# Optimization experiments

Measured on AMD Instinct MI355X. Metric: run time of the kernel, lower is better.

The kernel has to match this reference:

```python
import jax, jax.numpy as jnp
import numpy as np

EPS = 1.1920929e-07  # torch F.rms_norm default eps for fp32
HEADS = 16
KV_HEADS = 4
HEAD_DIM = 64
WINDOW = 1024
NEG = -1e30

def rms_norm(x):
    return x * jax.lax.rsqrt(jnp.mean(x * x, axis=-1, keepdims=True) + EPS)

def rope_freqs(L, head_dim):
    half = head_dim // 2
    inv_freq = 1.0 / (10000.0 ** (jnp.arange(half, dtype=jnp.float32) / half))
    f = jnp.outer(jnp.arange(L, dtype=jnp.float32), inv_freq)  # (L, half)
    return jnp.concatenate([f, f], axis=-1)  # (L, head_dim)

def apply_rope(x, freqs):
    # x: (B, L, H, D), freqs: (L, D)
    cos = jnp.cos(freqs)[None, :, None, :]
    sin = jnp.sin(freqs)[None, :, None, :]
    half = x.shape[-1] // 2
    x1, x2 = x[..., :half], x[..., half:]
    return jnp.concatenate([
        x1 * cos[..., :half] - x2 * sin[..., half:],
        x1 * sin[..., :half] + x2 * cos[..., half:],
    ], axis=-1)

def setup_inputs() -> dict:
    key = jax.random.key(0)
    k1, k2, k3, k4 = jax.random.split(key, 4)
    B, L, D = 2, 2048, 1024
    x = jax.random.normal(k1, (B, L, D), dtype=jnp.float32)
    w_qkv = jax.random.normal(k2, (1536, D), dtype=jnp.float32) * 0.02
    w_out = jax.random.normal(k3, (D, D), dtype=jnp.float32) * 0.02
    reset_mask = jax.random.randint(k4, (B, L), 0, 2) == 1
    return {"x": x, "w_qkv": w_qkv, "w_out": w_out, "reset_mask": reset_mask}

def reference(x, w_qkv, w_out, reset_mask):
    B, L, D = x.shape
    residual = x
    h = rms_norm(x)
    qkv = h @ w_qkv.T  # (B, L, 1536)
    q_dim = HEADS * HEAD_DIM
    kv_dim = KV_HEADS * HEAD_DIM
    q = qkv[..., :q_dim].reshape(B, L, HEADS, HEAD_DIM)
    k = qkv[..., q_dim:q_dim + kv_dim].reshape(B, L, KV_HEADS, HEAD_DIM)
    v = qkv[..., q_dim + kv_dim:].reshape(B, L, KV_HEADS, HEAD_DIM)
    q = rms_norm(q)
    k = rms_norm(k)
    freqs = rope_freqs(L, HEAD_DIM)
    q = apply_rope(q, freqs)
    k = apply_rope(k, freqs)
    groups = HEADS // KV_HEADS
    k = jnp.repeat(k, groups, axis=2)  # (B, L, H, D)
    v = jnp.repeat(v, groups, axis=2)
    q = q.transpose(0, 2, 1, 3)  # (B, H, L, D)
    k = k.transpose(0, 2, 1, 3)
    v = v.transpose(0, 2, 1, 3)
    # mask: same document & causal & sliding window
    seg = jnp.cumsum(reset_mask.astype(jnp.int32), axis=1)  # (B, L)
    same_doc = seg[:, :, None] == seg[:, None, :]  # (B, L, L)
    idx = jnp.arange(L)
    dist = idx[:, None] - idx[None, :]
    cw = (dist >= 0) & (dist < WINDOW)  # (L, L)
    mask = same_doc & cw[None]  # (B, L, L)
    scale = 1.0 / np.sqrt(HEAD_DIM)
    scores = jnp.einsum('bhqd,bhkd->bhqk', q, k) * scale
    scores = jnp.where(mask[:, None, :, :], scores, NEG)
    probs = jax.nn.softmax(scores, axis=-1)
    y = jnp.einsum('bhqk,bhkd->bhqd', probs, v)
    y = y.transpose(0, 2, 1, 3).reshape(B, L, D)
    return residual + y @ w_out.T
```

## Files before the change

### kernel.cpp

```cpp
#include <hip/hip_runtime.h>

typedef __attribute__((ext_vector_type(8))) short short8;
typedef __attribute__((ext_vector_type(4))) float f32x4;
typedef __attribute__((ext_vector_type(4))) unsigned short us4;

typedef unsigned int __attribute__((address_space(3))) lds_u32;
typedef const unsigned int __attribute__((address_space(1))) glb_u32;

__device__ __forceinline__ unsigned short f2bf(float f){
  unsigned int u = __float_as_uint(f);
  u = (u + 0x7FFFu + ((u >> 16) & 1u)) >> 16;
  return (unsigned short)u;
}
__device__ __forceinline__ float bf2f(unsigned short h){
  return __uint_as_float(((unsigned int)h) << 16);
}

__global__ __launch_bounds__(256)
void prep(const float* __restrict__ wq, const float* __restrict__ wo,
          unsigned short* __restrict__ wqb, unsigned short* __restrict__ wob,
          const float* __restrict__ x, unsigned short* __restrict__ h,
          const unsigned char* __restrict__ mb, int* __restrict__ lo){
  int blk = blockIdx.x;
  int t = threadIdx.x;
  if (blk < 2560) {
    int i = blk * 256 + t;
    const int n1 = 1536 * 1024 / 4;
    float4 v = (i < n1) ? ((const float4*)wq)[i] : ((const float4*)wo)[i - n1];
    us4 o = { f2bf(v.x), f2bf(v.y), f2bf(v.z), f2bf(v.w) };
    if (i < n1) ((us4*)wqb)[i] = o;
    else        ((us4*)wob)[i - n1] = o;
    return;
  }
  if (blk < 2560 + 4096) {
    int row = blk - 2560;
    float4 v = ((const float4*)(x + (size_t)row * 1024))[t];
    float ss = v.x*v.x + v.y*v.y + v.z*v.z + v.w*v.w;
    #pragma unroll
    for (int m = 1; m < 64; m <<= 1) ss += __shfl_xor(ss, m);
    __shared__ float wsum[4];
    if ((t & 63) == 0) wsum[t >> 6] = ss;
    __syncthreads();
    float tot = wsum[0] + wsum[1] + wsum[2] + wsum[3];
    float sc = rsqrtf(tot * (1.f/1024.f) + 1.1920929e-07f);
    us4 o = { f2bf(v.x*sc), f2bf(v.y*sc), f2bf(v.z*sc), f2bf(v.w*sc) };
    *(us4*)(h + (size_t)row * 1024 + t * 4) = o;
    return;
  }
  int b = blk - 2560 - 4096;
  __shared__ int flag_s;
  if (t == 0) flag_s = 0;
  __syncthreads();
  if (t < 64 && (t & 3) != 0 && mb[t] != 0) atomicOr(&flag_s, 1);
  __syncthreads();
  const bool isb = (flag_s != 0);
  const int* mi = (const int*)mb;
  int tmax = 0;
  int mvals[8];
  #pragma unroll
  for (int j = 0; j < 8; j++) {
    int p = t * 8 + j;
    int mv = isb ? (int)mb[b*2048 + p] : mi[b*2048 + p];
    mvals[j] = mv;
    if (mv) tmax = p;
  }
  __shared__ int sm[256];
  sm[t] = tmax;
  __syncthreads();
  for (int offd = 1; offd < 256; offd <<= 1) {
    int v = (t >= offd) ? sm[t - offd] : 0;
    __syncthreads();
    if (t >= offd) sm[t] = max(sm[t], v);
    __syncthreads();
  }
  int run = (t > 0) ? sm[t - 1] : 0;
  #pragma unroll
  for (int j = 0; j < 8; j++) {
    int p = t * 8 + j;
    if (mvals[j]) run = p;
    int l = run, wlo = p - 1023;
    if (wlo > l) l = wlo;
    if (l < 0) l = 0;
    lo[b*2048 + p] = l;
  }
}

template<bool BF_OUT, bool RES>
__global__ __launch_bounds__(256)
void gemm_nt(const unsigned short* __restrict__ A, const unsigned short* __restrict__ B,
             int M, int N, int K, float* __restrict__ Cf, unsigned short* __restrict__ Cb,
             const float* __restrict__ resid){
  __shared__ __align__(16) short As[128 * 64];
  __shared__ __align__(16) short Bs[128 * 64];
  const int nbn = N >> 7;
  const int bm = blockIdx.x / nbn;
  const int bn = blockIdx.x % nbn;
  const int t = threadIdx.x;
  const int lane = t & 63;
  const int wv = t >> 6;
  const int wm = (wv >> 1) * 64, wn = (wv & 1) * 64;
  const int lr = lane & 15, lg = lane >> 4;
  const int l8 = lane >> 3;
  const int c8 = (lane & 7) * 8;

  f32x4 acc[4][4];
  #pragma unroll
  for (int m = 0; m < 4; m++)
    #pragma unroll
    for (int n = 0; n < 4; n++) acc[m][n] = (f32x4){0.f,0.f,0.f,0.f};

  const unsigned short* Ab = A + (size_t)(bm * 128) * K;
  const unsigned short* Bb = B + (size_t)(bn * 128) * K;

  for (int kt = 0; kt < K; kt += 64) {
    #pragma unroll
    for (int i = 0; i < 4; i++) {
      int chunk = wv * 4 + i;
      int row = chunk * 8 + l8;
      __builtin_amdgcn_global_load_lds((glb_u32*)(Ab + (size_t)row * K + kt + c8),
                                       (lds_u32*)&As[chunk * 512], 16, 0, 0);
      __builtin_amdgcn_global_load_lds((glb_u32*)(Bb + (size_t)row * K + kt + c8),
                                       (lds_u32*)&Bs[chunk * 512], 16, 0, 0);
    }
    __syncthreads();
    #pragma unroll
    for (int kk = 0; kk < 2; kk++) {
      short8 af[4], bfr[4];
      #pragma unroll
      for (int m = 0; m < 4; m++) af[m] = *(const short8*)&As[(wm + m*16 + lr)*64 + kk*32 + lg*8];
      #pragma unroll
      for (int n = 0; n < 4; n++) bfr[n] = *(const short8*)&Bs[(wn + n*16 + lr)*64 + kk*32 + lg*8];
      #pragma unroll
      for (int m = 0; m < 4; m++)
        #pragma unroll
        for (int n = 0; n < 4; n++)
          acc[m][n] = __builtin_amdgcn_mfma_f32_16x16x32_bf16(af[m], bfr[n], acc[m][n], 0, 0, 0);
    }
    __syncthreads();
  }
  #pragma unroll
  for (int m = 0; m < 4; m++)
    #pragma unroll
    for (int n = 0; n < 4; n++)
      #pragma unroll
      for (int r = 0; r < 4; r++) {
        int grow = bm*128 + wm + m*16 + lg*4 + r;
        int gcol = bn*128 + wn + n*16 + lr;
        size_t idx = (size_t)grow * N + gcol;
        if (BF_OUT) { Cb[idx] = f2bf(acc[m][n][r]); }
        else {
          float v = acc[m][n][r];
          if (RES) v += resid[idx];
          Cf[idx] = v;
        }
      }
}

__global__ __launch_bounds__(256)
void post_qkv(const unsigned short* __restrict__ qkv,
              unsigned short* __restrict__ Qb, unsigned short* __restrict__ Kb,
              unsigned short* __restrict__ Vt){
  int w = blockIdx.x * 4 + (threadIdx.x >> 6);
  int lane = threadIdx.x & 63;
  int head = w % 24;
  int row  = w / 24;
  int b = row >> 11, pos = row & 2047;
  int off = head < 16 ? head * 64 : (head < 20 ? 1024 + (head-16)*64 : 1280 + (head-20)*64);
  float val = bf2f(qkv[(size_t)row * 1536 + off + lane]);
  if (head < 20) {
    float ss = val * val;
    #pragma unroll
    for (int m = 1; m < 64; m <<= 1) ss += __shfl_xor(ss, m);
    val *= rsqrtf(ss * (1.f/64.f) + 1.1920929e-07f);
    float part = __shfl_xor(val, 32);
    int i = lane & 31;
    float f = (float)pos * exp2f((float)i * (-13.287712379549449f / 32.f));
    float s, c; sincosf(f, &s, &c);
    val = (lane < 32) ? (val * c - part * s) : (part * s + val * c);
  }
  unsigned short o = f2bf(val);
  if (head < 16)      Qb[((size_t)((b*16 + head     )*2048 + pos))*64 + lane] = o;
  else if (head < 20) Kb[((size_t)((b*4  + head - 16)*2048 + pos))*64 + lane] = o;
  else                Vt[((size_t)((b*4  + head - 20)*64 + lane))*2048 + pos] = o;
}

__global__ __launch_bounds__(256)
void attn(const unsigned short* __restrict__ Qb, const unsigned short* __restrict__ Kb,
          const unsigned short* __restrict__ Vt, const int* __restrict__ lo,
          unsigned short* __restrict__ Y){
  int blk = blockIdx.x;
  int qt = blk & 31, h = (blk >> 5) & 15, b = blk >> 9;
  int wv = threadIdx.x >> 6, lane = threadIdx.x & 63;
  int lr = lane & 15, lg = lane >> 4;
  int q0 = qt * 64 + wv * 16;
  const unsigned short* Qh = Qb + ((size_t)(b*16 + h)) * 2048 * 64;
  int kvh = h >> 2;
  const unsigned short* Kh = Kb + ((size_t)(b*4 + kvh)) * 2048 * 64;
  const unsigned short* Vh = Vt + ((size_t)(b*4 + kvh)) * 64 * 2048;
  short8 qa0 = *(const short8*)(Qh + (size_t)(q0 + lr) * 64 + lg * 8);
  short8 qa1 = *(const short8*)(Qh + (size_t)(q0 + lr) * 64 + 32 + lg * 8);
  const int* lop = lo + b * 2048 + q0;
  int4 mlv = *(const int4*)(lop + lg * 4);
  int mylo[4] = {mlv.x, mlv.y, mlv.z, mlv.w};
  int kc0 = lop[0] & ~31;
  int kend = q0 + 15;
  f32x4 oacc[4];
  #pragma unroll
  for (int n = 0; n < 4; n++) oacc[n] = (f32x4){0.f,0.f,0.f,0.f};
  float den[4] = {0.f,0.f,0.f,0.f};
  __shared__ __align__(16) short Pl[4][16 * 40];
  short* Pw = Pl[wv];
  for (int kc = kc0; kc <= kend; kc += 32) {
    f32x4 s[2];
    #pragma unroll
    for (int n = 0; n < 2; n++) {
      int kr = kc + n*16 + lr;
      int krl = min(kr, 2047);
      short8 k0 = *(const short8*)(Kh + (size_t)krl * 64 + lg * 8);
      short8 k1 = *(const short8*)(Kh + (size_t)krl * 64 + 32 + lg * 8);
      f32x4 z = (f32x4){0.f,0.f,0.f,0.f};
      z = __builtin_amdgcn_mfma_f32_16x16x32_bf16(qa0, k0, z, 0, 0, 0);
      z = __builtin_amdgcn_mfma_f32_16x16x32_bf16(qa1, k1, z, 0, 0, 0);
      s[n] = z;
    }
    #pragma unroll
    for (int n = 0; n < 2; n++)
      #pragma unroll
      for (int r = 0; r < 4; r++) {
        int krow = kc + n*16 + lr;
        int qrow = q0 + lg*4 + r;
        bool valid = (krow >= mylo[r]) && (krow <= qrow);
        float p = valid ? __expf(s[n][r] * 0.125f) : 0.f;
        den[r] += p;
        Pw[(lg*4 + r) * 40 + n*16 + lr] = (short)f2bf(p);
      }
    short8 pa = *(const short8*)&Pw[lr * 40 + lg * 8];
    int vc = min(kc + lg * 8, 2040);
    #pragma unroll
    for (int n = 0; n < 4; n++) {
      short8 vb = *(const short8*)(Vh + (size_t)(n*16 + lr) * 2048 + vc);
      oacc[n] = __builtin_amdgcn_mfma_f32_16x16x32_bf16(pa, vb, oacc[n], 0, 0, 0);
    }
  }
  #pragma unroll
  for (int r = 0; r < 4; r++)
    #pragma unroll
    for (int m = 1; m < 16; m <<= 1) den[r] += __shfl_xor(den[r], m);
  #pragma unroll
  for (int n = 0; n < 4; n++)
    #pragma unroll
    for (int r = 0; r < 4; r++) {
      int qrow = q0 + lg*4 + r;
      Y[((size_t)(b*2048 + qrow)) * 1024 + h*64 + n*16 + lr] = f2bf(oacc[n][r] / den[r]);
    }
}

extern "C" void kernel_launch(void* const* d_in, const int* in_sizes, int n_in,
                              void* d_out, int out_size, void* d_ws, size_t ws_size,
                              hipStream_t stream){
  const float* x    = (const float*)d_in[0];
  const float* wqkv = (const float*)d_in[1];
  const float* wout = (const float*)d_in[2];
  const unsigned char* mask = (const unsigned char*)d_in[3];
  float* out = (float*)d_out;
  char* ws = (char*)d_ws;
  size_t off = 0;
  auto alloc = [&](size_t bytes) -> void* {
    void* p = ws + off;
    off += (bytes + 255) & ~(size_t)255;
    return p;
  };
  unsigned short* wq_b  = (unsigned short*)alloc((size_t)1536*1024*2);
  unsigned short* wo_b  = (unsigned short*)alloc((size_t)1024*1024*2);
  unsigned short* h_b   = (unsigned short*)alloc((size_t)4096*1024*2);
  unsigned short* qkv_b = (unsigned short*)alloc((size_t)4096*1536*2);
  unsigned short* q_b   = (unsigned short*)alloc((size_t)4096*1024*2);
  unsigned short* k_b   = (unsigned short*)alloc((size_t)4096*256*2);
  unsigned short* vt_b  = (unsigned short*)alloc((size_t)4096*256*2);
  unsigned short* y_b   = (unsigned short*)alloc((size_t)4096*1024*2);
  int* lo               = (int*)alloc((size_t)4096*4);

  prep<<<2560 + 4096 + 2, 256, 0, stream>>>(wqkv, wout, wq_b, wo_b, x, h_b, mask, lo);
  gemm_nt<true,  false><<<32*12, 256, 0, stream>>>(h_b, wq_b, 4096, 1536, 1024, nullptr, qkv_b, nullptr);
  post_qkv<<<24576, 256, 0, stream>>>(qkv_b, q_b, k_b, vt_b);
  attn<<<1024, 256, 0, stream>>>(q_b, k_b, vt_b, lo, y_b);
  gemm_nt<false, true><<<32*8, 256, 0, stream>>>(y_b, wo_b, 4096, 1024, 1024, out, nullptr, x);
}
```

Before: 164.8 us.

## Fuse QK norm, RoPE and V transpose into pipelined 128x64 QKV GEMM epilogue

Replaces the 128x128 GEMM with a 128x64-tile GEMM that double-buffers LDS loads with explicit waitcnt/barrier scheduling, adds an occupancy hint and swizzles block order. The QKV GEMM epilogue now applies per-head RMS norm and RoPE directly and writes Q/K in head-major layout and V transposed through a swizzled LDS buffer. This removes the separate post_qkv kernel and the intermediate qkv buffer round trip. The smaller tiles raise block count, but each block reuses less data and the epilogue does more work, including a per-row sincos.

```diff
diff --git a/kernel.cpp b/kernel.cpp
--- a/kernel.cpp
+++ b/kernel.cpp
@@ -85,103 +85,154 @@
   }
 }
 
-template<bool BF_OUT, bool RES>
-__global__ __launch_bounds__(256)
-void gemm_nt(const unsigned short* __restrict__ A, const unsigned short* __restrict__ B,
-             int M, int N, int K, float* __restrict__ Cf, unsigned short* __restrict__ Cb,
-             const float* __restrict__ resid){
-  __shared__ __align__(16) short As[128 * 64];
-  __shared__ __align__(16) short Bs[128 * 64];
-  const int nbn = N >> 7;
-  const int bm = blockIdx.x / nbn;
-  const int bn = blockIdx.x % nbn;
-  const int t = threadIdx.x;
-  const int lane = t & 63;
-  const int wv = t >> 6;
-  const int wm = (wv >> 1) * 64, wn = (wv & 1) * 64;
+template<int MODE>
+__global__ __launch_bounds__(256, 3)
+void gemm64(const unsigned short* __restrict__ A, const unsigned short* __restrict__ Bw,
+            unsigned short* __restrict__ Qb, unsigned short* __restrict__ Kb,
+            unsigned short* __restrict__ Vt, float* __restrict__ Cf,
+            const float* __restrict__ resid){
+  constexpr int K = 1024;
+  constexpr int NBN = (MODE == 0) ? 24 : 16;
+  __shared__ __align__(16) short As[2][128 * 64];
+  __shared__ __align__(16) short Bs[2][64 * 64];
+  const int cpx = (NBN * 32) >> 3;
+  const int swz = (blockIdx.x & 7) * cpx + (blockIdx.x >> 3);
+  const int bm = swz / NBN, bn = swz % NBN;
+  const int t = threadIdx.x, lane = t & 63, wv = t >> 6;
   const int lr = lane & 15, lg = lane >> 4;
-  const int l8 = lane >> 3;
-  const int c8 = (lane & 7) * 8;
-
-  f32x4 acc[4][4];
-  #pragma unroll
-  for (int m = 0; m < 4; m++)
+  const int l8 = lane >> 3, c8 = (lane & 7) * 8;
+  const int wr0 = wv * 32;
+
+  f32x4 acc[2][4];
+  #pragma unroll
+  for (int m = 0; m < 2; m++)
     #pragma unroll
     for (int n = 0; n < 4; n++) acc[m][n] = (f32x4){0.f,0.f,0.f,0.f};
 
   const unsigned short* Ab = A + (size_t)(bm * 128) * K;
-  const unsigned short* Bb = B + (size_t)(bn * 128) * K;
-
-  for (int kt = 0; kt < K; kt += 64) {
-    #pragma unroll
-    for (int i = 0; i < 4; i++) {
-      int chunk = wv * 4 + i;
-      int row = chunk * 8 + l8;
-      __builtin_amdgcn_global_load_lds((glb_u32*)(Ab + (size_t)row * K + kt + c8),
-                                       (lds_u32*)&As[chunk * 512], 16, 0, 0);
-      __builtin_amdgcn_global_load_lds((glb_u32*)(Bb + (size_t)row * K + kt + c8),
-                                       (lds_u32*)&Bs[chunk * 512], 16, 0, 0);
-    }
-    __syncthreads();
+  const unsigned short* Bb = Bw + (size_t)(bn * 64) * K;
+
+  #define STAGE(buf, kt) do { \
+    _Pragma("unroll") \
+    for (int i = 0; i < 6; i++) { \
+      int c = wv * 6 + i; \
+      if (c < 16) { \
+        __builtin_amdgcn_global_load_lds((glb_u32*)(Ab + (size_t)(c*8 + l8) * K + (kt) + c8), \
+                                         (lds_u32*)&As[buf][c * 512], 16, 0, 0); \
+      } else { \
+        __builtin_amdgcn_global_load_lds((glb_u32*)(Bb + (size_t)((c-16)*8 + l8) * K + (kt) + c8), \
+                                         (lds_u32*)&Bs[buf][(c-16) * 512], 16, 0, 0); \
+      } \
+    } \
+  } while (0)
+
+  auto COMPUTE = [&](int buf) {
     #pragma unroll
     for (int kk = 0; kk < 2; kk++) {
-      short8 af[4], bfr[4];
-      #pragma unroll
-      for (int m = 0; m < 4; m++) af[m] = *(const short8*)&As[(wm + m*16 + lr)*64 + kk*32 + lg*8];
-      #pragma unroll
-      for (int n = 0; n < 4; n++) bfr[n] = *(const short8*)&Bs[(wn + n*16 + lr)*64 + kk*32 + lg*8];
-      #pragma unroll
-      for (int m = 0; m < 4; m++)
+      short8 af[2], bfr[4];
+      #pragma unroll
+      for (int m = 0; m < 2; m++) af[m] = *(const short8*)&As[buf][(wr0 + m*16 + lr)*64 + kk*32 + lg*8];
+      #pragma unroll
+      for (int n = 0; n < 4; n++) bfr[n] = *(const short8*)&Bs[buf][(n*16 + lr)*64 + kk*32 + lg*8];
+      #pragma unroll
+      for (int m = 0; m < 2; m++)
         #pragma unroll
         for (int n = 0; n < 4; n++)
           acc[m][n] = __builtin_amdgcn_mfma_f32_16x16x32_bf16(af[m], bfr[n], acc[m][n], 0, 0, 0);
     }
+  };
+
+  const int nt = K >> 6;
+  STAGE(0, 0);
+  #pragma unroll 1
+  for (int tt = 0; tt < nt - 1; ++tt) {
+    int cur = tt & 1;
+    STAGE(cur ^ 1, (tt + 1) * 64);
+    __builtin_amdgcn_sched_barrier(0);
+    asm volatile("s_waitcnt vmcnt(6)" ::: "memory");
+    __builtin_amdgcn_s_barrier();
+    __builtin_amdgcn_sched_barrier(0);
+    COMPUTE(cur);
+    __builtin_amdgcn_sched_barrier(0);
+    __builtin_amdgcn_s_barrier();
+  }
+  asm volatile("s_waitcnt vmcnt(0)" ::: "memory");
+  __builtin_amdgcn_s_barrier();
+  __builtin_amdgcn_sched_barrier(0);
+  COMPUTE((nt - 1) & 1);
+  #undef STAGE
+
+  if constexpr (MODE == 1) {
+    #pragma unroll
+    for (int m = 0; m < 2; m++)
+      #pragma unroll
+      for (int n = 0; n < 4; n++)
+        #pragma unroll
+        for (int r = 0; r < 4; r++) {
+          int grow = bm*128 + wr0 + m*16 + lg*4 + r;
+          int gcol = bn*64 + n*16 + lr;
+          size_t idx = (size_t)grow * 1024 + gcol;
+          Cf[idx] = acc[m][n][r] + resid[idx];
+        }
+  } else if (bn < 20) {
+    const float cexp = -13.287712379549449f / 32.f;
+    const float if0 = exp2f((float)lr * cexp);
+    const float if1 = exp2f((float)(lr + 16) * cexp);
+    #pragma unroll
+    for (int m = 0; m < 2; m++)
+      #pragma unroll
+      for (int r = 0; r < 4; r++) {
+        float rs = acc[m][0][r]*acc[m][0][r] + acc[m][1][r]*acc[m][1][r]
+                 + acc[m][2][r]*acc[m][2][r] + acc[m][3][r]*acc[m][3][r];
+        #pragma unroll
+        for (int msk = 1; msk < 16; msk <<= 1) rs += __shfl_xor(rs, msk);
+        float sc = rsqrtf(rs * (1.f/64.f) + 1.1920929e-07f);
+        int grow = bm*128 + wr0 + m*16 + lg*4 + r;
+        int b = grow >> 11, pos = grow & 2047;
+        float th0 = (float)pos * if0, th1 = (float)pos * if1;
+        float s0, c0, s1, c1;
+        sincosf(th0, &s0, &c0);
+        sincosf(th1, &s1, &c1);
+        float v0 = acc[m][0][r]*sc, v1 = acc[m][1][r]*sc;
+        float v2 = acc[m][2][r]*sc, v3 = acc[m][3][r]*sc;
+        float o0 = v0*c0 - v2*s0;
+        float o1 = v1*c1 - v3*s1;
+        float o2 = v2*c0 + v0*s0;
+        float o3 = v3*c1 + v1*s1;
+        unsigned short* dst = (bn < 16)
+          ? Qb + ((size_t)((b*16 + bn)      * 2048 + pos)) * 64
+          : Kb + ((size_t)((b*4  + bn - 16) * 2048 + pos)) * 64;
+        dst[lr]      = f2bf(o0);
+        dst[16 + lr] = f2bf(o1);
+        dst[32 + lr] = f2bf(o2);
+        dst[48 + lr] = f2bf(o3);
+      }
+  } else {
+    short* Vl = &As[0][0];
+    #pragma unroll
+    for (int m = 0; m < 2; m++)
+      #pragma unroll
+      for (int n = 0; n < 4; n++)
+        #pragma unroll
+        for (int r = 0; r < 4; r++) {
+          int pl = wr0 + m*16 + lg*4 + r;
+          int d = n*16 + lr;
+          Vl[pl * 64 + (d ^ ((pl & 7) << 3))] = (short)f2bf(acc[m][n][r]);
+        }
     __syncthreads();
-  }
-  #pragma unroll
-  for (int m = 0; m < 4; m++)
-    #pragma unroll
-    for (int n = 0; n < 4; n++)
-      #pragma unroll
-      for (int r = 0; r < 4; r++) {
-        int grow = bm*128 + wm + m*16 + lg*4 + r;
-        int gcol = bn*128 + wn + n*16 + lr;
-        size_t idx = (size_t)grow * N + gcol;
-        if (BF_OUT) { Cb[idx] = f2bf(acc[m][n][r]); }
-        else {
-          float v = acc[m][n][r];
-          if (RES) v += resid[idx];
-          Cf[idx] = v;
-        }
-      }
-}
-
-__global__ __launch_bounds__(256)
-void post_qkv(const unsigned short* __restrict__ qkv,
-              unsigned short* __restrict__ Qb, unsigned short* __restrict__ Kb,
-              unsigned short* __restrict__ Vt){
-  int w = blockIdx.x * 4 + (threadIdx.x >> 6);
-  int lane = threadIdx.x & 63;
-  int head = w % 24;
-  int row  = w / 24;
-  int b = row >> 11, pos = row & 2047;
-  int off = head < 16 ? head * 64 : (head < 20 ? 1024 + (head-16)*64 : 1280 + (head-20)*64);
-  float val = bf2f(qkv[(size_t)row * 1536 + off + lane]);
-  if (head < 20) {
-    float ss = val * val;
-    #pragma unroll
-    for (int m = 1; m < 64; m <<= 1) ss += __shfl_xor(ss, m);
-    val *= rsqrtf(ss * (1.f/64.f) + 1.1920929e-07f);
-    float part = __shfl_xor(val, 32);
-    int i = lane & 31;
-    float f = (float)pos * exp2f((float)i * (-13.287712379549449f / 32.f));
-    float s, c; sincosf(f, &s, &c);
-    val = (lane < 32) ? (val * c - part * s) : (part * s + val * c);
-  }
-  unsigned short o = f2bf(val);
-  if (head < 16)      Qb[((size_t)((b*16 + head     )*2048 + pos))*64 + lane] = o;
-  else if (head < 20) Kb[((size_t)((b*4  + head - 16)*2048 + pos))*64 + lane] = o;
-  else                Vt[((size_t)((b*4  + head - 20)*64 + lane))*2048 + pos] = o;
+    int vh = bn - 20;
+    int b = bm >> 4;
+    int posg = (bm & 15) * 128;
+    int pl = (t & 63) * 2, dbase = (t >> 6) * 16;
+    #pragma unroll
+    for (int dd = 0; dd < 16; dd++) {
+      int d = dbase + dd;
+      unsigned short w0 = (unsigned short)Vl[pl * 64 + (d ^ ((pl & 7) << 3))];
+      unsigned short w1 = (unsigned short)Vl[(pl+1) * 64 + (d ^ (((pl+1) & 7) << 3))];
+      unsigned int pk = (unsigned int)w0 | ((unsigned int)w1 << 16);
+      *(unsigned int*)(Vt + ((size_t)((b*4 + vh)*64 + d)) * 2048 + posg + pl) = pk;
+    }
+  }
 }
 
 __global__ __launch_bounds__(256)
@@ -273,7 +324,6 @@
   unsigned short* wq_b  = (unsigned short*)alloc((size_t)1536*1024*2);
   unsigned short* wo_b  = (unsigned short*)alloc((size_t)1024*1024*2);
   unsigned short* h_b   = (unsigned short*)alloc((size_t)4096*1024*2);
-  unsigned short* qkv_b = (unsigned short*)alloc((size_t)4096*1536*2);
   unsigned short* q_b   = (unsigned short*)alloc((size_t)4096*1024*2);
   unsigned short* k_b   = (unsigned short*)alloc((size_t)4096*256*2);
   unsigned short* vt_b  = (unsigned short*)alloc((size_t)4096*256*2);
@@ -281,8 +331,7 @@
   int* lo               = (int*)alloc((size_t)4096*4);
 
   prep<<<2560 + 4096 + 2, 256, 0, stream>>>(wqkv, wout, wq_b, wo_b, x, h_b, mask, lo);
-  gemm_nt<true,  false><<<32*12, 256, 0, stream>>>(h_b, wq_b, 4096, 1536, 1024, nullptr, qkv_b, nullptr);
-  post_qkv<<<24576, 256, 0, stream>>>(qkv_b, q_b, k_b, vt_b);
+  gemm64<0><<<768, 256, 0, stream>>>(h_b, wq_b, q_b, k_b, vt_b, nullptr, nullptr);
   attn<<<1024, 256, 0, stream>>>(q_b, k_b, vt_b, lo, y_b);
-  gemm_nt<false, true><<<32*8, 256, 0, stream>>>(y_b, wo_b, 4096, 1024, 1024, out, nullptr, x);
-}
+  gemm64<1><<<512, 256, 0, stream>>>(y_b, wo_b, nullptr, nullptr, nullptr, out, x);
+}
```

New measurement: 145.7 us. -11.6%, faster.
